# Kernel optimization log

Hardware: AMD Instinct MI355X
Metric: run time of the kernel (lower is better)

The kernel has to match this reference:

```python
import jax, jax.numpy as jnp
import numpy as np

B, T, E = 2, 2048, 1024
H = 16
D = E // H  # head_dim = 64


def setup_inputs() -> dict:
    key = jax.random.key(0)
    k1, k2, k3 = jax.random.split(key, 3)
    x = jax.random.normal(k1, (B, T, E), dtype=jnp.float32)
    w_qkv = jax.random.normal(k2, (3 * E, E), dtype=jnp.float32) * 0.02
    w_proj = jax.random.normal(k3, (E, E), dtype=jnp.float32) * 0.02
    return {"x": x, "w_qkv": w_qkv, "w_proj": w_proj}


def reference(x, w_qkv, w_proj):
    b, t, c = x.shape
    # qkv projection (torch Linear: x @ W^T), split into q,k,v
    qkv = jnp.einsum('btc,fc->btf', x, w_qkv)  # [B,T,3E]
    q, k, v = jnp.split(qkv, 3, axis=-1)
    # [B,T,E] -> [B,H,T,D]
    q = q.reshape(b, t, H, D).transpose(0, 2, 1, 3)
    k = k.reshape(b, t, H, D).transpose(0, 2, 1, 3)
    v = v.reshape(b, t, H, D).transpose(0, 2, 1, 3)
    scale = 1.0 / jnp.sqrt(jnp.float32(D))
    att = jnp.einsum('bhqd,bhkd->bhqk', q, k) * scale  # [B,H,T,T]
    causal = jnp.tril(jnp.ones((t, t), dtype=bool))
    att = jnp.where(causal[None, None], att, -jnp.inf)
    att = jax.nn.softmax(att, axis=-1)
    out = jnp.einsum('bhqk,bhkd->bhqd', att, v)  # [B,H,T,D]
    out = out.transpose(0, 2, 1, 3).reshape(b, t, c)  # [B,T,E]
    out = jnp.einsum('btc,oc->bto', out, w_proj)
    return out
```

## Files before the change

kernel.cpp:

```cpp
#include <hip/hip_runtime.h>
#include <stdint.h>
#include <stddef.h>

typedef __attribute__((ext_vector_type(8))) short s16x8;
typedef __attribute__((ext_vector_type(4))) short s16x4;
typedef __attribute__((ext_vector_type(4))) float f32x4;

#define B_  2
#define T_  2048
#define E_  1024
#define H_  16
#define E3_ 3072

__device__ __forceinline__ short f2bf(float f) {
  union { float f; uint32_t u; } v; v.f = f;
  uint32_t u = v.u;
  return (short)((u + 0x7FFFu + ((u >> 16) & 1u)) >> 16);
}

__device__ __forceinline__ uint32_t fbits(float f) {
  union { float f; uint32_t u; } v; v.f = f; return v.u;
}

__device__ __forceinline__ void gload_lds16(const short* g, short* l) {
  __builtin_amdgcn_global_load_lds(
      (__attribute__((address_space(1))) void*)(const_cast<short*>(g)),
      (__attribute__((address_space(3))) void*)(l), 16, 0, 0);
}

__global__ void castk_all(const float* __restrict__ x, const float* __restrict__ wqkv,
                          const float* __restrict__ wproj, short* __restrict__ xb,
                          short* __restrict__ wqkvb, short* __restrict__ wprojb) {
  const int bid = blockIdx.x;
  const float* in; short* out; int i; float sc = 1.0f;
  if (bid < 4096)      { in = x;     out = xb;     i = bid * 256 + threadIdx.x; }
  else if (bid < 7168) { in = wqkv;  out = wqkvb;  i = (bid - 4096) * 256 + threadIdx.x;
                         if (i < 262144) sc = 0.18033688011112042f; }
  else                 { in = wproj; out = wprojb; i = (bid - 7168) * 256 + threadIdx.x; }
  const float4 v = ((const float4*)in)[i];
  s16x4 o;
  o[0] = f2bf(v.x * sc); o[1] = f2bf(v.y * sc);
  o[2] = f2bf(v.z * sc); o[3] = f2bf(v.w * sc);
  ((s16x4*)out)[i] = o;
}

template <int MODE>
__global__ void gemm_nt_128(const short* __restrict__ A, const short* __restrict__ B,
                            void* __restrict__ Cv, short* __restrict__ vt,
                            int M, int N, int K) {
  __shared__ short As[128 * 32];
  __shared__ short Bs[128 * 32];
  const int tid  = threadIdx.x;
  const int lane = tid & 63;
  const int w    = tid >> 6;
  const int quad = lane >> 4;
  const int l16  = lane & 15;
  const int wm   = (w >> 1) * 64;
  const int wn   = (w & 1) * 64;
  const int bm   = blockIdx.y * 128;
  const int bn   = blockIdx.x * 128;

  f32x4 acc[4][4];
#pragma unroll
  for (int i = 0; i < 4; i++)
#pragma unroll
    for (int j = 0; j < 4; j++) acc[i][j] = (f32x4){0.f, 0.f, 0.f, 0.f};

  const int srow = w * 32 + (lane >> 2);
  const int scol = (lane & 3) * 8;
  const short* gA = A + (size_t)(bm + srow) * K + scol;
  const short* gB = B + (size_t)(bn + srow) * K + scol;
  short* lA = As + (w * 32) * 32;
  short* lB = Bs + (w * 32) * 32;

  for (int k0 = 0; k0 < K; k0 += 32) {
    __syncthreads();
    gload_lds16(gA + k0,          lA);
    gload_lds16(gA + 16 * K + k0, lA + 16 * 32);
    gload_lds16(gB + k0,          lB);
    gload_lds16(gB + 16 * K + k0, lB + 16 * 32);
    __syncthreads();

    s16x8 a[4], b[4];
#pragma unroll
    for (int i = 0; i < 4; i++)
      a[i] = *(const s16x8*)&As[(wm + i * 16 + l16) * 32 + quad * 8];
#pragma unroll
    for (int j = 0; j < 4; j++)
      b[j] = *(const s16x8*)&Bs[(wn + j * 16 + l16) * 32 + quad * 8];
#pragma unroll
    for (int i = 0; i < 4; i++)
#pragma unroll
      for (int j = 0; j < 4; j++)
        acc[i][j] = __builtin_amdgcn_mfma_f32_16x16x32_bf16(a[i], b[j], acc[i][j], 0, 0, 0);
  }

  if (MODE == 2 && bn >= 2 * E_) {
#pragma unroll
    for (int i = 0; i < 4; i++) {
      const int token = bm + wm + i * 16 + quad * 4;
      const int bb = token >> 11, t = token & (T_ - 1);
#pragma unroll
      for (int j = 0; j < 4; j++) {
        const int col = bn + wn + j * 16 + l16 - 2 * E_;
        s16x4 pk;
#pragma unroll
        for (int r = 0; r < 4; r++) pk[r] = f2bf(acc[i][j][r]);
        *(s16x4*)&vt[((size_t)(bb * H_ + (col >> 6)) * 64 + (col & 63)) * T_ + t] = pk;
      }
    }
  } else {
#pragma unroll
    for (int i = 0; i < 4; i++) {
      const int row0 = bm + wm + i * 16 + quad * 4;
#pragma unroll
      for (int j = 0; j < 4; j++) {
        const int col = bn + wn + j * 16 + l16;
#pragma unroll
        for (int r = 0; r < 4; r++) {
          const size_t idx = (size_t)(row0 + r) * N + col;
          if (MODE == 2) ((short*)Cv)[idx] = f2bf(acc[i][j][r]);
          else           ((float*)Cv)[idx] = acc[i][j][r];
        }
      }
    }
  }
}

__global__ void __launch_bounds__(256, 4)
attn_kernel(const short* __restrict__ qkv, const short* __restrict__ vt,
            short* __restrict__ attout) {
  __shared__ short Ks[2][64 * 64];
  __shared__ short Vs[2][64 * 64];
  const int tid  = threadIdx.x;
  const int lane = tid & 63;
  const int w    = tid >> 6;
  const int quad = lane >> 4;
  const int l16  = lane & 15;
  const int bh = blockIdx.x;
  const int b = bh >> 4, h = bh & 15;
  const int ya = blockIdx.y & 7, yb = blockIdx.y >> 3;
  const int qt = (3 - yb) * 8 + ((yb & 1) ? ya : (7 - ya));
  const int q0b = qt * 64;
  const int q0w = q0b + w * 16;
  const float NEG_INF = -__builtin_inff();

  const int srl = lane >> 3;
  const int sgc = ((lane & 7) ^ srl) * 8;
  const short* gK = qkv + (size_t)(b * T_) * E3_ + E_ + h * 64 + sgc;
  const short* gV = vt + (size_t)(bh * 64) * T_ + sgc;
  const int swz = (l16 & 7);

  s16x8 ones;
#pragma unroll
  for (int i = 0; i < 8; i++) ones[i] = (short)0x3F80;

  auto stage = [&](int kv0s, int bf) {
#pragma unroll
    for (int i = 0; i < 2; i++) {
      const int r8 = w * 16 + i * 8;
      const int rowp = r8 + srl;
      const int rowk = (rowp & ~12) | ((rowp & 4) << 1) | ((rowp & 8) >> 1);
      gload_lds16(gK + (size_t)(kv0s + rowk) * E3_, &Ks[bf][r8 * 64]);
      gload_lds16(gV + (size_t)rowp * T_ + kv0s,    &Vs[bf][r8 * 64]);
    }
  };

  const short* qbase = qkv + (size_t)(b * T_ + q0w + l16) * E3_ + h * 64 + quad * 8;
  const s16x8 qf0 = *(const s16x8*)(qbase);
  const s16x8 qf1 = *(const s16x8*)(qbase + 32);

  f32x4 o[4]; f32x4 ol = (f32x4){0.f, 0.f, 0.f, 0.f};
#pragma unroll
  for (int j = 0; j < 4; j++) o[j] = (f32x4){0.f, 0.f, 0.f, 0.f};

  stage(0, 0);
  __syncthreads();

  for (int kv0 = 0, g = 0; kv0 <= q0b; kv0 += 64, g++) {
    const int cur = g & 1;

    s16x8 kf[2][4];
#pragma unroll
    for (int c = 0; c < 2; c++)
#pragma unroll
      for (int j = 0; j < 4; j++)
        kf[c][j] = *(const s16x8*)&Ks[cur][(j * 16 + l16) * 64 + (((c * 4 + quad) ^ swz) * 8)];

    if (kv0 + 64 <= q0b) stage(kv0 + 64, cur ^ 1);

    f32x4 s[4];
#pragma unroll
    for (int j = 0; j < 4; j++) s[j] = (f32x4){0.f, 0.f, 0.f, 0.f};
    __builtin_amdgcn_s_setprio(1);
#pragma unroll
    for (int c = 0; c < 2; c++)
#pragma unroll
      for (int j = 0; j < 4; j++)
        s[j] = __builtin_amdgcn_mfma_f32_16x16x32_bf16(kf[c][j], c == 0 ? qf0 : qf1, s[j], 0, 0, 0);
    __builtin_amdgcn_s_setprio(0);

    if (kv0 == q0b) {
      const int tq4 = ((quad & 1) << 3) | ((quad >> 1) << 2);
#pragma unroll
      for (int j = 0; j < 4; j++)
#pragma unroll
        for (int r = 0; r < 4; r++)
          if (j * 16 + tq4 + r > w * 16 + l16) s[j][r] = NEG_INF;
    }

#pragma unroll
    for (int j = 0; j < 4; j++) {
      s[j][0] = exp2f(s[j][0]); s[j][1] = exp2f(s[j][1]);
      s[j][2] = exp2f(s[j][2]); s[j][3] = exp2f(s[j][3]);
    }

    int dj[4][2];
#pragma unroll
    for (int j = 0; j < 4; j++) {
      asm("v_cvt_pk_bf16_f32 %0, %1, %2" : "=v"(dj[j][0]) : "v"(s[j][0]), "v"(s[j][1]));
      asm("v_cvt_pk_bf16_f32 %0, %1, %2" : "=v"(dj[j][1]) : "v"(s[j][2]), "v"(s[j][3]));
    }

    s16x8 F[2];
#pragma unroll
    for (int c = 0; c < 2; c++) {
      int x0 = dj[2 * c][0], y0 = dj[2 * c + 1][0];
      int x1 = dj[2 * c][1], y1 = dj[2 * c + 1][1];
      asm("v_permlane32_swap_b32 %0, %1" : "+v"(x0), "+v"(y0));
      asm("v_permlane32_swap_b32 %0, %1" : "+v"(x1), "+v"(y1));
      union { int i4[4]; s16x8 v; } u;
      u.i4[0] = x0; u.i4[1] = x1; u.i4[2] = y0; u.i4[3] = y1;
      F[c] = u.v;
    }

    __builtin_amdgcn_s_setprio(1);
#pragma unroll
    for (int c = 0; c < 2; c++) {
      ol = __builtin_amdgcn_mfma_f32_16x16x32_bf16(ones, F[c], ol, 0, 0, 0);
#pragma unroll
      for (int j = 0; j < 4; j++) {
        const s16x8 vf = *(const s16x8*)&Vs[cur][(j * 16 + l16) * 64 + (((c * 4 + quad) ^ swz) * 8)];
        o[j] = __builtin_amdgcn_mfma_f32_16x16x32_bf16(vf, F[c], o[j], 0, 0, 0);
      }
    }
    __builtin_amdgcn_s_setprio(0);

    __syncthreads();
  }

  const float inv = 1.0f / ol[0];
  const int q = q0w + l16;
  short* ob = attout + ((size_t)(b * T_ + q) * H_ + h) * 64 + quad * 4;
#pragma unroll
  for (int j = 0; j < 4; j++) {
    s16x4 pk;
#pragma unroll
    for (int r = 0; r < 4; r++) pk[r] = f2bf(o[j][r] * inv);
    *(s16x4*)&ob[16 * j] = pk;
  }
}

extern "C" void kernel_launch(void* const* d_in, const int* in_sizes, int n_in,
                              void* d_out, int out_size, void* d_ws, size_t ws_size,
                              hipStream_t stream) {
  const float* x     = (const float*)d_in[0];
  const float* wqkv  = (const float*)d_in[1];
  const float* wproj = (const float*)d_in[2];

  if (ws_size < 58720256u) return;
  short* ws     = (short*)d_ws;
  short* xb     = ws;
  short* wqkvb  = xb + 4194304;
  short* wprojb = wqkvb + 3145728;
  short* qkv    = wprojb + 1048576;
  short* vt     = qkv + 12582912;
  short* attb   = vt + 4194304;

  castk_all<<<8192, 256, 0, stream>>>(x, wqkv, wproj, xb, wqkvb, wprojb);
  gemm_nt_128<2><<<dim3(24, 32), 256, 0, stream>>>(xb, wqkvb, qkv, vt, 4096, 3072, 1024);
  attn_kernel<<<dim3(32, 32), 256, 0, stream>>>(qkv, vt, attb);
  gemm_nt_128<0><<<dim3(8, 32), 256, 0, stream>>>(attb, wprojb, d_out, nullptr, 4096, 1024, 1024);
}
```

Before: 167.7 us.

## Split attention work across waves by query pairs and key halves with LDS reduction

```diff
diff --git a/kernel.cpp b/kernel.cpp
--- a/kernel.cpp
+++ b/kernel.cpp
@@ -135,6 +135,8 @@
   const int tid  = threadIdx.x;
   const int lane = tid & 63;
   const int w    = tid >> 6;
+  const int wq   = w >> 1;
+  const int ws   = w & 1;
   const int quad = lane >> 4;
   const int l16  = lane & 15;
   const int bh = blockIdx.x;
@@ -142,7 +144,6 @@
   const int ya = blockIdx.y & 7, yb = blockIdx.y >> 3;
   const int qt = (3 - yb) * 8 + ((yb & 1) ? ya : (7 - ya));
   const int q0b = qt * 64;
-  const int q0w = q0b + w * 16;
   const float NEG_INF = -__builtin_inff();
 
   const int srl = lane >> 3;
@@ -166,13 +167,21 @@
     }
   };
 
-  const short* qbase = qkv + (size_t)(b * T_ + q0w + l16) * E3_ + h * 64 + quad * 8;
-  const s16x8 qf0 = *(const s16x8*)(qbase);
-  const s16x8 qf1 = *(const s16x8*)(qbase + 32);
-
-  f32x4 o[4]; f32x4 ol = (f32x4){0.f, 0.f, 0.f, 0.f};
-#pragma unroll
-  for (int j = 0; j < 4; j++) o[j] = (f32x4){0.f, 0.f, 0.f, 0.f};
+  s16x8 qf[2][2];
+#pragma unroll
+  for (int n = 0; n < 2; n++) {
+    const short* qbase = qkv + (size_t)(b * T_ + q0b + wq * 32 + n * 16 + l16) * E3_ + h * 64 + quad * 8;
+    qf[n][0] = *(const s16x8*)(qbase);
+    qf[n][1] = *(const s16x8*)(qbase + 32);
+  }
+
+  f32x4 o[2][4], ol[2];
+#pragma unroll
+  for (int n = 0; n < 2; n++) {
+    ol[n] = (f32x4){0.f, 0.f, 0.f, 0.f};
+#pragma unroll
+    for (int j = 0; j < 4; j++) o[n][j] = (f32x4){0.f, 0.f, 0.f, 0.f};
+  }
 
   stage(0, 0);
   __syncthreads();
@@ -180,84 +189,108 @@
   for (int kv0 = 0, g = 0; kv0 <= q0b; kv0 += 64, g++) {
     const int cur = g & 1;
 
-    s16x8 kf[2][4];
-#pragma unroll
-    for (int c = 0; c < 2; c++)
+    if (kv0 + 64 <= q0b) stage(kv0 + 64, cur ^ 1);
+
+    const bool diag = (kv0 == q0b);
+    if (!(diag && ws > wq)) {
+      s16x8 kf[2][2];
+#pragma unroll
+      for (int c = 0; c < 2; c++)
+#pragma unroll
+        for (int j = 0; j < 2; j++)
+          kf[c][j] = *(const s16x8*)&Ks[cur][(ws * 32 + j * 16 + l16) * 64 + (((c * 4 + quad) ^ swz) * 8)];
+
+      f32x4 s[2][2];
+#pragma unroll
+      for (int n = 0; n < 2; n++)
+#pragma unroll
+        for (int j = 0; j < 2; j++) s[n][j] = (f32x4){0.f, 0.f, 0.f, 0.f};
+
+      __builtin_amdgcn_s_setprio(1);
+#pragma unroll
+      for (int c = 0; c < 2; c++)
+#pragma unroll
+        for (int n = 0; n < 2; n++)
+#pragma unroll
+          for (int j = 0; j < 2; j++)
+            s[n][j] = __builtin_amdgcn_mfma_f32_16x16x32_bf16(kf[c][j], qf[n][c], s[n][j], 0, 0, 0);
+      __builtin_amdgcn_s_setprio(0);
+
+      if (diag && ws == wq) {
+        const int tq4 = ((quad & 1) << 3) | ((quad >> 1) << 2);
+#pragma unroll
+        for (int n = 0; n < 2; n++)
+#pragma unroll
+          for (int j = 0; j < 2; j++)
+#pragma unroll
+            for (int r = 0; r < 4; r++)
+              if (j * 16 + tq4 + r > n * 16 + l16) s[n][j][r] = NEG_INF;
+      }
+
+      s16x8 F[2];
+#pragma unroll
+      for (int n = 0; n < 2; n++) {
+#pragma unroll
+        for (int j = 0; j < 2; j++) {
+          s[n][j][0] = exp2f(s[n][j][0]); s[n][j][1] = exp2f(s[n][j][1]);
+          s[n][j][2] = exp2f(s[n][j][2]); s[n][j][3] = exp2f(s[n][j][3]);
+        }
+        int x0, x1, y0, y1;
+        asm("v_cvt_pk_bf16_f32 %0, %1, %2" : "=v"(x0) : "v"(s[n][0][0]), "v"(s[n][0][1]));
+        asm("v_cvt_pk_bf16_f32 %0, %1, %2" : "=v"(x1) : "v"(s[n][0][2]), "v"(s[n][0][3]));
+        asm("v_cvt_pk_bf16_f32 %0, %1, %2" : "=v"(y0) : "v"(s[n][1][0]), "v"(s[n][1][1]));
+        asm("v_cvt_pk_bf16_f32 %0, %1, %2" : "=v"(y1) : "v"(s[n][1][2]), "v"(s[n][1][3]));
+        asm("v_permlane32_swap_b32 %0, %1" : "+v"(x0), "+v"(y0));
+        asm("v_permlane32_swap_b32 %0, %1" : "+v"(x1), "+v"(y1));
+        union { int i4[4]; s16x8 v; } u;
+        u.i4[0] = x0; u.i4[1] = x1; u.i4[2] = y0; u.i4[3] = y1;
+        F[n] = u.v;
+      }
+
+      __builtin_amdgcn_s_setprio(1);
+#pragma unroll
+      for (int n = 0; n < 2; n++)
+        ol[n] = __builtin_amdgcn_mfma_f32_16x16x32_bf16(ones, F[n], ol[n], 0, 0, 0);
+#pragma unroll
+      for (int j = 0; j < 4; j++) {
+        const s16x8 vf = *(const s16x8*)&Vs[cur][(j * 16 + l16) * 64 + (((ws * 4 + quad) ^ swz) * 8)];
+#pragma unroll
+        for (int n = 0; n < 2; n++)
+          o[n][j] = __builtin_amdgcn_mfma_f32_16x16x32_bf16(vf, F[n], o[n][j], 0, 0, 0);
+      }
+      __builtin_amdgcn_s_setprio(0);
+    }
+
+    __syncthreads();
+  }
+
+  float* red  = (float*)&Ks[0][0];
+  float* redl = (float*)&Vs[0][0];
+  if (ws == 1) {
+#pragma unroll
+    for (int n = 0; n < 2; n++) {
 #pragma unroll
       for (int j = 0; j < 4; j++)
-        kf[c][j] = *(const s16x8*)&Ks[cur][(j * 16 + l16) * 64 + (((c * 4 + quad) ^ swz) * 8)];
-
-    if (kv0 + 64 <= q0b) stage(kv0 + 64, cur ^ 1);
-
-    f32x4 s[4];
-#pragma unroll
-    for (int j = 0; j < 4; j++) s[j] = (f32x4){0.f, 0.f, 0.f, 0.f};
-    __builtin_amdgcn_s_setprio(1);
-#pragma unroll
-    for (int c = 0; c < 2; c++)
-#pragma unroll
-      for (int j = 0; j < 4; j++)
-        s[j] = __builtin_amdgcn_mfma_f32_16x16x32_bf16(kf[c][j], c == 0 ? qf0 : qf1, s[j], 0, 0, 0);
-    __builtin_amdgcn_s_setprio(0);
-
-    if (kv0 == q0b) {
-      const int tq4 = ((quad & 1) << 3) | ((quad >> 1) << 2);
-#pragma unroll
-      for (int j = 0; j < 4; j++)
-#pragma unroll
-        for (int r = 0; r < 4; r++)
-          if (j * 16 + tq4 + r > w * 16 + l16) s[j][r] = NEG_INF;
-    }
-
-#pragma unroll
-    for (int j = 0; j < 4; j++) {
-      s[j][0] = exp2f(s[j][0]); s[j][1] = exp2f(s[j][1]);
-      s[j][2] = exp2f(s[j][2]); s[j][3] = exp2f(s[j][3]);
-    }
-
-    int dj[4][2];
-#pragma unroll
-    for (int j = 0; j < 4; j++) {
-      asm("v_cvt_pk_bf16_f32 %0, %1, %2" : "=v"(dj[j][0]) : "v"(s[j][0]), "v"(s[j][1]));
-      asm("v_cvt_pk_bf16_f32 %0, %1, %2" : "=v"(dj[j][1]) : "v"(s[j][2]), "v"(s[j][3]));
-    }
-
-    s16x8 F[2];
-#pragma unroll
-    for (int c = 0; c < 2; c++) {
-      int x0 = dj[2 * c][0], y0 = dj[2 * c + 1][0];
-      int x1 = dj[2 * c][1], y1 = dj[2 * c + 1][1];
-      asm("v_permlane32_swap_b32 %0, %1" : "+v"(x0), "+v"(y0));
-      asm("v_permlane32_swap_b32 %0, %1" : "+v"(x1), "+v"(y1));
-      union { int i4[4]; s16x8 v; } u;
-      u.i4[0] = x0; u.i4[1] = x1; u.i4[2] = y0; u.i4[3] = y1;
-      F[c] = u.v;
-    }
-
-    __builtin_amdgcn_s_setprio(1);
-#pragma unroll
-    for (int c = 0; c < 2; c++) {
-      ol = __builtin_amdgcn_mfma_f32_16x16x32_bf16(ones, F[c], ol, 0, 0, 0);
+        *(f32x4*)&red[((wq * 2 + n) * 4 + j) * 256 + lane * 4] = o[n][j];
+      redl[(wq * 2 + n) * 64 + lane] = ol[n][0];
+    }
+  }
+  __syncthreads();
+  if (ws == 0) {
+#pragma unroll
+    for (int n = 0; n < 2; n++) {
+      const float inv = 1.0f / (ol[n][0] + redl[(wq * 2 + n) * 64 + lane]);
+      const int q = q0b + wq * 32 + n * 16 + l16;
+      short* ob = attout + ((size_t)(b * T_ + q) * H_ + h) * 64 + quad * 4;
 #pragma unroll
       for (int j = 0; j < 4; j++) {
-        const s16x8 vf = *(const s16x8*)&Vs[cur][(j * 16 + l16) * 64 + (((c * 4 + quad) ^ swz) * 8)];
-        o[j] = __builtin_amdgcn_mfma_f32_16x16x32_bf16(vf, F[c], o[j], 0, 0, 0);
-      }
-    }
-    __builtin_amdgcn_s_setprio(0);
-
-    __syncthreads();
-  }
-
-  const float inv = 1.0f / ol[0];
-  const int q = q0w + l16;
-  short* ob = attout + ((size_t)(b * T_ + q) * H_ + h) * 64 + quad * 4;
-#pragma unroll
-  for (int j = 0; j < 4; j++) {
-    s16x4 pk;
-#pragma unroll
-    for (int r = 0; r < 4; r++) pk[r] = f2bf(o[j][r] * inv);
-    *(s16x4*)&ob[16 * j] = pk;
+        const f32x4 t = *(const f32x4*)&red[((wq * 2 + n) * 4 + j) * 256 + lane * 4];
+        s16x4 pk;
+#pragma unroll
+        for (int r = 0; r < 4; r++) pk[r] = f2bf((o[n][j][r] + t[r]) * inv);
+        *(s16x4*)&ob[16 * j] = pk;
+      }
+    }
   }
 }
 
```

Measured after the change: 172.8 us. 1.03x slower.

## Load K and V fragments directly from global memory, dropping LDS staging

Applied to the files above, without the earlier changes.

```diff
diff --git a/kernel.cpp b/kernel.cpp
--- a/kernel.cpp
+++ b/kernel.cpp
@@ -130,8 +130,6 @@
 __global__ void __launch_bounds__(256, 4)
 attn_kernel(const short* __restrict__ qkv, const short* __restrict__ vt,
             short* __restrict__ attout) {
-  __shared__ short Ks[2][64 * 64];
-  __shared__ short Vs[2][64 * 64];
   const int tid  = threadIdx.x;
   const int lane = tid & 63;
   const int w    = tid >> 6;
@@ -145,26 +143,14 @@
   const int q0w = q0b + w * 16;
   const float NEG_INF = -__builtin_inff();
 
-  const int srl = lane >> 3;
-  const int sgc = ((lane & 7) ^ srl) * 8;
-  const short* gK = qkv + (size_t)(b * T_) * E3_ + E_ + h * 64 + sgc;
-  const short* gV = vt + (size_t)(bh * 64) * T_ + sgc;
-  const int swz = (l16 & 7);
+  const int sl16 = (l16 & 3) | ((l16 & 4) << 1) | ((l16 & 8) >> 1);
+
+  const short* gKr = qkv + ((size_t)(b * T_) + sl16) * E3_ + E_ + h * 64 + quad * 8;
+  const short* gVr = vt + ((size_t)(bh * 64) + l16) * T_ + quad * 8;
 
   s16x8 ones;
 #pragma unroll
   for (int i = 0; i < 8; i++) ones[i] = (short)0x3F80;
-
-  auto stage = [&](int kv0s, int bf) {
-#pragma unroll
-    for (int i = 0; i < 2; i++) {
-      const int r8 = w * 16 + i * 8;
-      const int rowp = r8 + srl;
-      const int rowk = (rowp & ~12) | ((rowp & 4) << 1) | ((rowp & 8) >> 1);
-      gload_lds16(gK + (size_t)(kv0s + rowk) * E3_, &Ks[bf][r8 * 64]);
-      gload_lds16(gV + (size_t)rowp * T_ + kv0s,    &Vs[bf][r8 * 64]);
-    }
-  };
 
   const short* qbase = qkv + (size_t)(b * T_ + q0w + l16) * E3_ + h * 64 + quad * 8;
   const s16x8 qf0 = *(const s16x8*)(qbase);
@@ -174,20 +160,15 @@
 #pragma unroll
   for (int j = 0; j < 4; j++) o[j] = (f32x4){0.f, 0.f, 0.f, 0.f};
 
-  stage(0, 0);
-  __syncthreads();
-
-  for (int kv0 = 0, g = 0; kv0 <= q0b; kv0 += 64, g++) {
-    const int cur = g & 1;
-
+#pragma unroll 1
+  for (int kv0 = 0; kv0 <= q0b; kv0 += 64) {
+    const short* kp = gKr + (size_t)kv0 * E3_;
     s16x8 kf[2][4];
 #pragma unroll
     for (int c = 0; c < 2; c++)
 #pragma unroll
       for (int j = 0; j < 4; j++)
-        kf[c][j] = *(const s16x8*)&Ks[cur][(j * 16 + l16) * 64 + (((c * 4 + quad) ^ swz) * 8)];
-
-    if (kv0 + 64 <= q0b) stage(kv0 + 64, cur ^ 1);
+        kf[c][j] = *(const s16x8*)(kp + (size_t)(j * 16) * E3_ + c * 32);
 
     f32x4 s[4];
 #pragma unroll
@@ -234,19 +215,18 @@
       F[c] = u.v;
     }
 
+    const short* vp = gVr + kv0;
     __builtin_amdgcn_s_setprio(1);
 #pragma unroll
     for (int c = 0; c < 2; c++) {
       ol = __builtin_amdgcn_mfma_f32_16x16x32_bf16(ones, F[c], ol, 0, 0, 0);
 #pragma unroll
       for (int j = 0; j < 4; j++) {
-        const s16x8 vf = *(const s16x8*)&Vs[cur][(j * 16 + l16) * 64 + (((c * 4 + quad) ^ swz) * 8)];
+        const s16x8 vf = *(const s16x8*)(vp + (size_t)(j * 16) * T_ + c * 32);
         o[j] = __builtin_amdgcn_mfma_f32_16x16x32_bf16(vf, F[c], o[j], 0, 0, 0);
       }
     }
     __builtin_amdgcn_s_setprio(0);
-
-    __syncthreads();
   }
 
   const float inv = 1.0f / ol[0];
```

Result: slower. 258.0 us (+53.8%).

## Split long causal attention query tiles across two blocks with a merge kernel

Applied to the files above, without the earlier changes.

```diff
diff --git a/kernel.cpp b/kernel.cpp
--- a/kernel.cpp
+++ b/kernel.cpp
@@ -16,10 +16,6 @@
   union { float f; uint32_t u; } v; v.f = f;
   uint32_t u = v.u;
   return (short)((u + 0x7FFFu + ((u >> 16) & 1u)) >> 16);
-}
-
-__device__ __forceinline__ uint32_t fbits(float f) {
-  union { float f; uint32_t u; } v; v.f = f; return v.u;
 }
 
 __device__ __forceinline__ void gload_lds16(const short* g, short* l) {
@@ -127,9 +123,22 @@
   }
 }
 
-__global__ void __launch_bounds__(256, 4)
-attn_kernel(const short* __restrict__ qkv, const short* __restrict__ vt,
-            short* __restrict__ attout) {
+__device__ const unsigned char aorder[48] = {
+  15, 63, 95, 62,
+  14, 94, 61, 93, 60,
+  13, 92, 59, 91, 58,
+  12, 90, 57, 89, 56,
+  11, 88, 55, 87, 54,
+  10, 86, 53, 85, 52,
+   9, 84, 51, 83, 50,
+   8, 82, 49, 81, 48,
+   7, 80,
+   6,  5,  4,  3,  2,  1,  0
+};
+
+__global__ void __launch_bounds__(256, 5)
+attn_kernel(short* qkv, const short* __restrict__ vt,
+            short* __restrict__ attout, float* __restrict__ scr) {
   __shared__ short Ks[2][64 * 64];
   __shared__ short Vs[2][64 * 64];
   const int tid  = threadIdx.x;
@@ -137,12 +146,14 @@
   const int w    = tid >> 6;
   const int quad = lane >> 4;
   const int l16  = lane & 15;
-  const int bh = blockIdx.x;
+  const int bh = blockIdx.x & 31;
   const int b = bh >> 4, h = bh & 15;
-  const int ya = blockIdx.y & 7, yb = blockIdx.y >> 3;
-  const int qt = (3 - yb) * 8 + ((yb & 1) ? ya : (7 - ya));
-  const int q0b = qt * 64;
-  const int q0w = q0b + w * 16;
+  const int e = aorder[blockIdx.x >> 5];
+  const int qt = e & 31, kind = e >> 5;
+  const int hq = (qt + 2) >> 1;
+  const int t0 = (kind == 2) ? hq : 0;
+  const int t1 = (kind == 1) ? (hq - 1) : qt;
+  const int q0w = qt * 64 + w * 16;
   const float NEG_INF = -__builtin_inff();
 
   const int srl = lane >> 3;
@@ -174,10 +185,10 @@
 #pragma unroll
   for (int j = 0; j < 4; j++) o[j] = (f32x4){0.f, 0.f, 0.f, 0.f};
 
-  stage(0, 0);
+  stage(t0 * 64, 0);
   __syncthreads();
 
-  for (int kv0 = 0, g = 0; kv0 <= q0b; kv0 += 64, g++) {
+  for (int t = t0, g = 0; t <= t1; t++, g++) {
     const int cur = g & 1;
 
     s16x8 kf[2][4];
@@ -187,7 +198,7 @@
       for (int j = 0; j < 4; j++)
         kf[c][j] = *(const s16x8*)&Ks[cur][(j * 16 + l16) * 64 + (((c * 4 + quad) ^ swz) * 8)];
 
-    if (kv0 + 64 <= q0b) stage(kv0 + 64, cur ^ 1);
+    if (t + 1 <= t1) stage((t + 1) * 64, cur ^ 1);
 
     f32x4 s[4];
 #pragma unroll
@@ -200,7 +211,7 @@
         s[j] = __builtin_amdgcn_mfma_f32_16x16x32_bf16(kf[c][j], c == 0 ? qf0 : qf1, s[j], 0, 0, 0);
     __builtin_amdgcn_s_setprio(0);
 
-    if (kv0 == q0b) {
+    if (t == qt) {
       const int tq4 = ((quad & 1) << 3) | ((quad >> 1) << 2);
 #pragma unroll
       for (int j = 0; j < 4; j++)
@@ -249,16 +260,50 @@
     __syncthreads();
   }
 
-  const float inv = 1.0f / ol[0];
-  const int q = q0w + l16;
-  short* ob = attout + ((size_t)(b * T_ + q) * H_ + h) * 64 + quad * 4;
-#pragma unroll
-  for (int j = 0; j < 4; j++) {
-    s16x4 pk;
-#pragma unroll
-    for (int r = 0; r < 4; r++) pk[r] = f2bf(o[j][r] * inv);
-    *(s16x4*)&ob[16 * j] = pk;
+  if (kind == 0) {
+    const float inv = 1.0f / ol[0];
+    const int q = q0w + l16;
+    short* ob = attout + ((size_t)(b * T_ + q) * H_ + h) * 64 + quad * 4;
+#pragma unroll
+    for (int j = 0; j < 4; j++) {
+      s16x4 pk;
+#pragma unroll
+      for (int r = 0; r < 4; r++) pk[r] = f2bf(o[j][r] * inv);
+      *(s16x4*)&ob[16 * j] = pk;
+    }
+  } else {
+    const int q  = q0w + l16;
+    const int qi = q - 1024;
+    float* sp = scr + (kind == 2 ? 2097152 : 0)
+                    + ((size_t)(bh * 1024 + qi)) * 64 + quad * 4;
+#pragma unroll
+    for (int j = 0; j < 4; j++) *(f32x4*)&sp[16 * j] = o[j];
+    if (quad == 0) {
+      float* lp = (float*)(qkv + (size_t)(b * T_ + q) * E3_ + 2 * E_);
+      lp[h + (kind == 2 ? 16 : 0)] = ol[0];
+    }
   }
+}
+
+__global__ void att_norm(const float* __restrict__ scr, const short* __restrict__ qkv,
+                         short* __restrict__ attb) {
+  const int bid = blockIdx.x;
+  const int bh2 = bid & 31;
+  const int g   = bid >> 5;
+  const int tid = threadIdx.x;
+  const int qi  = g * 16 + (tid >> 4);
+  const int d0  = (tid & 15) * 4;
+  const int b = bh2 >> 4, h = bh2 & 15;
+  const size_t idx = ((size_t)bh2 * 1024 + qi) * 64 + d0;
+  const f32x4 a = *(const f32x4*)&scr[idx];
+  const f32x4 c = *(const f32x4*)&scr[2097152 + idx];
+  const float* lp = (const float*)(qkv + (size_t)(b * T_ + 1024 + qi) * E3_ + 2 * E_);
+  const float inv = 1.0f / (lp[h] + lp[16 + h]);
+  short* ob = attb + ((size_t)(b * T_ + 1024 + qi) * H_ + h) * 64 + d0;
+  s16x4 pk;
+#pragma unroll
+  for (int r = 0; r < 4; r++) pk[r] = f2bf((a[r] + c[r]) * inv);
+  *(s16x4*)ob = pk;
 }
 
 extern "C" void kernel_launch(void* const* d_in, const int* in_sizes, int n_in,
@@ -279,6 +324,7 @@
 
   castk_all<<<8192, 256, 0, stream>>>(x, wqkv, wproj, xb, wqkvb, wprojb);
   gemm_nt_128<2><<<dim3(24, 32), 256, 0, stream>>>(xb, wqkvb, qkv, vt, 4096, 3072, 1024);
-  attn_kernel<<<dim3(32, 32), 256, 0, stream>>>(qkv, vt, attb);
+  attn_kernel<<<dim3(1536), 256, 0, stream>>>(qkv, vt, attb, (float*)d_out);
+  att_norm<<<dim3(2048), 256, 0, stream>>>((const float*)d_out, qkv, attb);
   gemm_nt_128<0><<<dim3(8, 32), 256, 0, stream>>>(attb, wprojb, d_out, nullptr, 4096, 1024, 1024);
 }
```

After: 174.3 us. 1.04x slower.
